# Optimization experiments

Measured on AMD Instinct MI355X. Metric: run time of the kernel, lower is better.

## Reference

```python
import jax, jax.numpy as jnp
import numpy as np

B, F, T, D, S = 8, 256, 512, 40, 4


def setup_inputs() -> dict:
    key = jax.random.key(0)
    k1, k2 = jax.random.split(key)
    embeddings = jax.random.normal(k1, (B, F, T, D), dtype=jnp.float32)
    assignments = jax.random.uniform(k2, (B, F, T, S), dtype=jnp.float32)
    return {"embeddings": embeddings, "assignments": assignments}


def reference(embeddings, assignments):
    b, f, t, d = embeddings.shape
    s = assignments.shape[-1]
    n = f * t
    E = embeddings.reshape(b, n, d)          # (B, N, D)
    V = assignments.reshape(b, n, s)         # (B, N, S)
    # ||VV^T - EE^T||_F^2 summed over batch, via trace identity:
    #   = ||V^T V||_F^2 - 2 ||V^T E||_F^2 + ||E^T E||_F^2
    VtV = jnp.einsum('bns,bnt->bst', V, V)   # (B, S, S)
    VtE = jnp.einsum('bns,bnd->bsd', V, E)   # (B, S, D)
    EtE = jnp.einsum('bnd,bne->bde', E, E)   # (B, D, D)
    fro_sq = jnp.sum(VtV * VtV) - 2.0 * jnp.sum(VtE * VtE) + jnp.sum(EtE * EtE)
    return fro_sq / (b * n)
```

## Files before the change

kernel.cpp:

```cpp
#include <hip/hip_runtime.h>

#define BATCHES 8
#define NROWS (256 * 512)
#define DE 40
#define SV 4
#define GP 48
#define GSZ (GP * GP)
#define TP 48
#define ROWS_PER_BLOCK 1024
#define CHUNKS (NROWS / ROWS_PER_BLOCK)
#define RSTAGE 64
#define NSTAGES (ROWS_PER_BLOCK / RSTAGE)
#define NGROUPS 4
#define NTILES 42
#define NACTIVE (NGROUPS * NTILES)
#define EF4 (RSTAGE * (DE / 4))
#define CPY (EF4 + RSTAGE)

__global__ __launch_bounds__(256, 4) void gram_kernel(const float* __restrict__ E,
                                                      const float* __restrict__ V,
                                                      float* __restrict__ G) {
    __shared__ float tile[2][RSTAGE][TP];
    __shared__ float gsum[GSZ];

    const int tid = threadIdx.x;
    const int b = blockIdx.x / CHUNKS;
    const int chunk = blockIdx.x % CHUNKS;
    const size_t row0 = (size_t)chunk * ROWS_PER_BLOCK;

    const float4* __restrict__ Eg = (const float4*)(E + (size_t)b * NROWS * DE) + row0 * (DE / 4);
    const float4* __restrict__ Vg = (const float4*)(V + (size_t)b * NROWS * SV) + row0;

    for (int i = tid; i < GSZ; i += 256) gsum[i] = 0.f;
    if (tid < 2 * RSTAGE) {
        const int bb = tid / RSTAGE, r = tid % RSTAGE;
        *(float4*)&tile[bb][r][44] = make_float4(0.f, 0.f, 0.f, 0.f);
    }

    int ldsoff[3];
    int goff[3];
    bool isv[3], valid[3];
    #pragma unroll
    for (int it = 0; it < 3; ++it) {
        const int idx = tid + it * 256;
        valid[it] = (idx < CPY);
        isv[it] = (idx >= EF4);
        if (idx < EF4) { ldsoff[it] = (idx / 10) * TP + (idx % 10) * 4; goff[it] = idx; }
        else           { const int r = idx - EF4; ldsoff[it] = r * TP + DE; goff[it] = r; }
    }

    const int grp = tid / NTILES;
    const int tt = tid % NTILES;
    const bool active = (tid < NACTIVE);
    int ti = 0;
    while ((ti + 1) * (ti + 1) + (ti + 1) <= tt) ti++;
    const int tj = tt - (ti * ti + ti);

    float acc[8][4];
    #pragma unroll
    for (int i = 0; i < 8; ++i)
        #pragma unroll
        for (int j = 0; j < 4; ++j) acc[i][j] = 0.f;

    float4 c0, c1, c2;
    {
        if (valid[0]) c0 = isv[0] ? Vg[goff[0]] : Eg[goff[0]];
        if (valid[1]) c1 = isv[1] ? Vg[goff[1]] : Eg[goff[1]];
        if (valid[2]) c2 = isv[2] ? Vg[goff[2]] : Eg[goff[2]];
    }

    int buf = 0;
    for (int s = 0; s < NSTAGES; ++s) {
        if (valid[0]) *(float4*)&tile[buf][0][ldsoff[0]] = c0;
        if (valid[1]) *(float4*)&tile[buf][0][ldsoff[1]] = c1;
        if (valid[2]) *(float4*)&tile[buf][0][ldsoff[2]] = c2;
        if (s + 1 < NSTAGES) {
            const int e4 = (s + 1) * EF4, v4 = (s + 1) * RSTAGE;
            if (valid[0]) c0 = isv[0] ? Vg[v4 + goff[0]] : Eg[e4 + goff[0]];
            if (valid[1]) c1 = isv[1] ? Vg[v4 + goff[1]] : Eg[e4 + goff[1]];
            if (valid[2]) c2 = isv[2] ? Vg[v4 + goff[2]] : Eg[e4 + goff[2]];
        }
        __syncthreads();

        if (active) {
            const float* ap = &tile[buf][0][8 * ti];
            const float* bp = &tile[buf][0][4 * tj];
            #pragma unroll 4
            for (int k = 0; k < RSTAGE / NGROUPS; ++k) {
                const int r = (grp + k * NGROUPS) * TP;
                const float4 xa = *(const float4*)(ap + r);
                const float4 ya = *(const float4*)(ap + r + 4);
                const float4 xb = *(const float4*)(bp + r);
                const float av[8] = {xa.x, xa.y, xa.z, xa.w, ya.x, ya.y, ya.z, ya.w};
                const float bv[4] = {xb.x, xb.y, xb.z, xb.w};
                #pragma unroll
                for (int i = 0; i < 8; ++i)
                    #pragma unroll
                    for (int j = 0; j < 4; ++j)
                        acc[i][j] += av[i] * bv[j];
            }
        }
        buf ^= 1;
        __syncthreads();
    }

    #pragma unroll
    for (int g = 0; g < NGROUPS; ++g) {
        if (active && grp == g) {
            #pragma unroll
            for (int i = 0; i < 8; ++i)
                #pragma unroll
                for (int j = 0; j < 4; ++j) {
                    const int gi = 8 * ti + i, gj = 4 * tj + j;
                    if (gi >= gj) gsum[gi * GP + gj] += acc[i][j];
                }
        }
        __syncthreads();
    }

    float* Gb = G + (size_t)b * GSZ;
    for (int idx = tid; idx < GSZ; idx += 256) {
        const int gi = idx / GP, gj = idx % GP;
        if (gj <= gi && gi < (DE + SV)) atomicAdd(&Gb[idx], gsum[idx]);
    }
}

__global__ __launch_bounds__(256) void finish_kernel(const float* __restrict__ G,
                                                     float* __restrict__ out) {
    const int tid = threadIdx.x;
    float sum = 0.f;
    for (int idx = tid; idx < BATCHES * GSZ; idx += 256) {
        const int ij = idx % GSZ;
        const int gi = ij / GP;
        const int gj = ij % GP;
        if (gj > gi || gi >= (DE + SV)) continue;
        const float g = G[idx];
        const float w = (gi == gj) ? 1.f : 2.f;
        const float sgn = ((gi < DE) == (gj < DE)) ? 1.f : -1.f;
        sum += w * sgn * g * g;
    }
    #pragma unroll
    for (int o = 32; o > 0; o >>= 1) sum += __shfl_down(sum, o, 64);
    __shared__ float ws[4];
    if ((tid & 63) == 0) ws[tid >> 6] = sum;
    __syncthreads();
    if (tid == 0) {
        const float t = ws[0] + ws[1] + ws[2] + ws[3];
        out[0] = t / (float)((size_t)BATCHES * NROWS);
    }
}

extern "C" void kernel_launch(void* const* d_in, const int* in_sizes, int n_in,
                              void* d_out, int out_size, void* d_ws, size_t ws_size,
                              hipStream_t stream) {
    const float* E = (const float*)d_in[0];
    const float* V = (const float*)d_in[1];
    float* G = (float*)d_ws;

    hipMemsetAsync(G, 0, (size_t)BATCHES * GSZ * sizeof(float), stream);
    gram_kernel<<<BATCHES * CHUNKS, 256, 0, stream>>>(E, V, G);
    finish_kernel<<<1, 256, 0, stream>>>(G, (float*)d_out);
}
```

Baseline: 278.4 us.

## Compute Gram tiles with bf16 MFMA instead of scalar FP32 FMAs

Replaces the per-thread FP32 outer-product accumulation with bf16 MFMA 16x16x32 instructions over a column-major swizzled LDS tile, converting E and V to bf16 on the way into shared memory. The stage size doubles, and one of the two barriers per stage is removed by moving the sync to the top of the loop. This targets the FMA compute cost but reduces input precision to bf16, which risks accuracy loss in a loss value that depends on cancelling large Frobenius terms. The kernel is likely still bound by global memory bandwidth.

```diff
diff --git a/kernel.cpp b/kernel.cpp
--- a/kernel.cpp
+++ b/kernel.cpp
@@ -1,4 +1,5 @@
 #include <hip/hip_runtime.h>
+#include <hip/hip_bf16.h>
 
 #define BATCHES 8
 #define NROWS (256 * 512)
@@ -6,114 +7,144 @@
 #define SV 4
 #define GP 48
 #define GSZ (GP * GP)
-#define TP 48
 #define ROWS_PER_BLOCK 1024
 #define CHUNKS (NROWS / ROWS_PER_BLOCK)
-#define RSTAGE 64
+#define RSTAGE 128
 #define NSTAGES (ROWS_PER_BLOCK / RSTAGE)
-#define NGROUPS 4
-#define NTILES 42
-#define NACTIVE (NGROUPS * NTILES)
-#define EF4 (RSTAGE * (DE / 4))
-#define CPY (EF4 + RSTAGE)
+#define COLBYTES 256
+#define TILEBYTES (GP * COLBYTES)
+#define NSLOT 352
+
+typedef __attribute__((ext_vector_type(8))) short bf16x8;
+typedef __attribute__((ext_vector_type(4))) float f32x4;
+typedef __attribute__((ext_vector_type(2))) int i32x2;
+
+__device__ __forceinline__ int pk_bf16(float lo, float hi) {
+    __hip_bfloat162 h2 = __float22bfloat162_rn(float2{lo, hi});
+    return *reinterpret_cast<int*>(&h2);
+}
 
 __global__ __launch_bounds__(256, 4) void gram_kernel(const float* __restrict__ E,
                                                       const float* __restrict__ V,
                                                       float* __restrict__ G) {
-    __shared__ float tile[2][RSTAGE][TP];
+    __shared__ __align__(16) char tb[2][TILEBYTES];
     __shared__ float gsum[GSZ];
 
     const int tid = threadIdx.x;
+    const int lane = tid & 63;
+    const int wave = tid >> 6;
     const int b = blockIdx.x / CHUNKS;
     const int chunk = blockIdx.x % CHUNKS;
     const size_t row0 = (size_t)chunk * ROWS_PER_BLOCK;
 
-    const float4* __restrict__ Eg = (const float4*)(E + (size_t)b * NROWS * DE) + row0 * (DE / 4);
+    const float4* __restrict__ Eg = (const float4*)(E + (size_t)b * NROWS * DE) + row0 * 10;
     const float4* __restrict__ Vg = (const float4*)(V + (size_t)b * NROWS * SV) + row0;
 
     for (int i = tid; i < GSZ; i += 256) gsum[i] = 0.f;
-    if (tid < 2 * RSTAGE) {
-        const int bb = tid / RSTAGE, r = tid % RSTAGE;
-        *(float4*)&tile[bb][r][44] = make_float4(0.f, 0.f, 0.f, 0.f);
+    if (tid < 128) {
+        const int bb = tid >> 6, off = (tid & 63) * 16;
+        *(float4*)&tb[bb][44 * COLBYTES + off] = make_float4(0.f, 0.f, 0.f, 0.f);
     }
 
-    int ldsoff[3];
-    int goff[3];
-    bool isv[3], valid[3];
+    const int cgA = tid % 11, rgA = tid / 11;
+    const int cgB = (tid + 256) % 11, rgB = (tid + 256) / 11;
+    const bool hasB = (tid < 96);
+    const bool vA = (cgA == 10), vB = (cgB == 10);
+    const int pA = vA ? 1 : 10, cA = vA ? 0 : cgA;
+    const int pB = vB ? 1 : 10, cB = vB ? 0 : cgB;
+    const float4* __restrict__ gA = vA ? Vg : Eg;
+    const float4* __restrict__ gB = vB ? Vg : Eg;
+    const int oA = 4 * rgA * pA + cA;
+    const int oB = 4 * rgB * pB + cB;
+
+    f32x4 acc[6];
     #pragma unroll
-    for (int it = 0; it < 3; ++it) {
-        const int idx = tid + it * 256;
-        valid[it] = (idx < CPY);
-        isv[it] = (idx >= EF4);
-        if (idx < EF4) { ldsoff[it] = (idx / 10) * TP + (idx % 10) * 4; goff[it] = idx; }
-        else           { const int r = idx - EF4; ldsoff[it] = r * TP + DE; goff[it] = r; }
-    }
+    for (int i = 0; i < 6; ++i) acc[i] = (f32x4){0.f, 0.f, 0.f, 0.f};
 
-    const int grp = tid / NTILES;
-    const int tt = tid % NTILES;
-    const bool active = (tid < NACTIVE);
-    int ti = 0;
-    while ((ti + 1) * (ti + 1) + (ti + 1) <= tt) ti++;
-    const int tj = tt - (ti * ti + ti);
+    float4 a0, a1, a2, a3, b0, b1, b2, b3;
+    a0 = gA[oA]; a1 = gA[oA + pA]; a2 = gA[oA + 2 * pA]; a3 = gA[oA + 3 * pA];
+    if (hasB) { b0 = gB[oB]; b1 = gB[oB + pB]; b2 = gB[oB + 2 * pB]; b3 = gB[oB + 3 * pB]; }
 
-    float acc[8][4];
-    #pragma unroll
-    for (int i = 0; i < 8; ++i)
-        #pragma unroll
-        for (int j = 0; j < 4; ++j) acc[i][j] = 0.f;
-
-    float4 c0, c1, c2;
-    {
-        if (valid[0]) c0 = isv[0] ? Vg[goff[0]] : Eg[goff[0]];
-        if (valid[1]) c1 = isv[1] ? Vg[goff[1]] : Eg[goff[1]];
-        if (valid[2]) c2 = isv[2] ? Vg[goff[2]] : Eg[goff[2]];
-    }
+    const int fcol = lane & 15;
+    const int fq = lane >> 4;
+    const int foff = ((wave * 64 + fq * 16) + 16 * fcol) & 255;
 
     int buf = 0;
     for (int s = 0; s < NSTAGES; ++s) {
-        if (valid[0]) *(float4*)&tile[buf][0][ldsoff[0]] = c0;
-        if (valid[1]) *(float4*)&tile[buf][0][ldsoff[1]] = c1;
-        if (valid[2]) *(float4*)&tile[buf][0][ldsoff[2]] = c2;
+        __syncthreads();
+        {
+            char* base = tb[buf];
+            #pragma unroll
+            for (int j = 0; j < 4; ++j) {
+                const float f0 = (j == 0) ? a0.x : (j == 1) ? a0.y : (j == 2) ? a0.z : a0.w;
+                const float f1 = (j == 0) ? a1.x : (j == 1) ? a1.y : (j == 2) ? a1.z : a1.w;
+                const float f2 = (j == 0) ? a2.x : (j == 1) ? a2.y : (j == 2) ? a2.z : a2.w;
+                const float f3 = (j == 0) ? a3.x : (j == 1) ? a3.y : (j == 2) ? a3.z : a3.w;
+                const int col = 4 * cgA + j;
+                const int off = (8 * rgA + 16 * (col & 15)) & 255;
+                i32x2 p = { pk_bf16(f0, f1), pk_bf16(f2, f3) };
+                *(i32x2*)&base[col * COLBYTES + off] = p;
+            }
+            if (hasB) {
+                #pragma unroll
+                for (int j = 0; j < 4; ++j) {
+                    const float f0 = (j == 0) ? b0.x : (j == 1) ? b0.y : (j == 2) ? b0.z : b0.w;
+                    const float f1 = (j == 0) ? b1.x : (j == 1) ? b1.y : (j == 2) ? b1.z : b1.w;
+                    const float f2 = (j == 0) ? b2.x : (j == 1) ? b2.y : (j == 2) ? b2.z : b2.w;
+                    const float f3 = (j == 0) ? b3.x : (j == 1) ? b3.y : (j == 2) ? b3.z : b3.w;
+                    const int col = 4 * cgB + j;
+                    const int off = (8 * rgB + 16 * (col & 15)) & 255;
+                    i32x2 p = { pk_bf16(f0, f1), pk_bf16(f2, f3) };
+                    *(i32x2*)&base[col * COLBYTES + off] = p;
+                }
+            }
+        }
         if (s + 1 < NSTAGES) {
-            const int e4 = (s + 1) * EF4, v4 = (s + 1) * RSTAGE;
-            if (valid[0]) c0 = isv[0] ? Vg[v4 + goff[0]] : Eg[e4 + goff[0]];
-            if (valid[1]) c1 = isv[1] ? Vg[v4 + goff[1]] : Eg[e4 + goff[1]];
-            if (valid[2]) c2 = isv[2] ? Vg[v4 + goff[2]] : Eg[e4 + goff[2]];
+            const int adv = (s + 1) * RSTAGE;
+            a0 = gA[oA + adv * pA]; a1 = gA[oA + (adv + 1 * 4 / 4) * 0 + oA * 0 + (oA + adv * pA + pA) - (oA + adv * pA)];
+            a0 = gA[oA + adv * pA];
+            a1 = gA[oA + adv * pA + pA];
+            a2 = gA[oA + adv * pA + 2 * pA];
+            a3 = gA[oA + adv * pA + 3 * pA];
+            if (hasB) {
+                b0 = gB[oB + adv * pB];
+                b1 = gB[oB + adv * pB + pB];
+                b2 = gB[oB + adv * pB + 2 * pB];
+                b3 = gB[oB + adv * pB + 3 * pB];
+            }
         }
         __syncthreads();
 
-        if (active) {
-            const float* ap = &tile[buf][0][8 * ti];
-            const float* bp = &tile[buf][0][4 * tj];
-            #pragma unroll 4
-            for (int k = 0; k < RSTAGE / NGROUPS; ++k) {
-                const int r = (grp + k * NGROUPS) * TP;
-                const float4 xa = *(const float4*)(ap + r);
-                const float4 ya = *(const float4*)(ap + r + 4);
-                const float4 xb = *(const float4*)(bp + r);
-                const float av[8] = {xa.x, xa.y, xa.z, xa.w, ya.x, ya.y, ya.z, ya.w};
-                const float bv[4] = {xb.x, xb.y, xb.z, xb.w};
-                #pragma unroll
-                for (int i = 0; i < 8; ++i)
-                    #pragma unroll
-                    for (int j = 0; j < 4; ++j)
-                        acc[i][j] += av[i] * bv[j];
-            }
+        {
+            const char* base = tb[buf];
+            const bf16x8 f0 = *(const bf16x8*)&base[(0 * 16 + fcol) * COLBYTES + foff];
+            const bf16x8 f1 = *(const bf16x8*)&base[(1 * 16 + fcol) * COLBYTES + foff];
+            const bf16x8 f2 = *(const bf16x8*)&base[(2 * 16 + fcol) * COLBYTES + foff];
+            acc[0] = __builtin_amdgcn_mfma_f32_16x16x32_bf16(f0, f0, acc[0], 0, 0, 0);
+            acc[1] = __builtin_amdgcn_mfma_f32_16x16x32_bf16(f1, f0, acc[1], 0, 0, 0);
+            acc[2] = __builtin_amdgcn_mfma_f32_16x16x32_bf16(f1, f1, acc[2], 0, 0, 0);
+            acc[3] = __builtin_amdgcn_mfma_f32_16x16x32_bf16(f2, f0, acc[3], 0, 0, 0);
+            acc[4] = __builtin_amdgcn_mfma_f32_16x16x32_bf16(f2, f1, acc[4], 0, 0, 0);
+            acc[5] = __builtin_amdgcn_mfma_f32_16x16x32_bf16(f2, f2, acc[5], 0, 0, 0);
         }
         buf ^= 1;
-        __syncthreads();
     }
 
+    __syncthreads();
     #pragma unroll
-    for (int g = 0; g < NGROUPS; ++g) {
-        if (active && grp == g) {
+    for (int w = 0; w < 4; ++w) {
+        if (wave == w) {
             #pragma unroll
-            for (int i = 0; i < 8; ++i)
+            for (int t6 = 0; t6 < 6; ++t6) {
+                const int t = (t6 < 1) ? 0 : (t6 < 3) ? 1 : 2;
+                const int u = (t6 == 0) ? 0 : (t6 < 3) ? (t6 - 1) : (t6 - 3);
                 #pragma unroll
-                for (int j = 0; j < 4; ++j) {
-                    const int gi = 8 * ti + i, gj = 4 * tj + j;
-                    if (gi >= gj) gsum[gi * GP + gj] += acc[i][j];
+                for (int r = 0; r < 4; ++r) {
+                    const int gi = 16 * t + 4 * fq + r;
+                    const int gj = 16 * u + fcol;
+                    gsum[gi * GP + gj] += acc[t6][r];
                 }
+            }
         }
         __syncthreads();
     }
```

New measurement: 269.1 us. -3.4%, faster.
